# Kernel optimization log

Measured on AMD Instinct MI355X. Metric: run time of the kernel, lower is better.

Reference implementation:

```python
import jax, jax.numpy as jnp
import numpy as np

B, L, H = 2, 2048, 1024
N_HEADS = 16
HEAD = H // N_HEADS
LN_EPS = 1e-12


def setup_inputs() -> dict:
    key = jax.random.key(0)
    ks = jax.random.split(key, 8)
    s = 1.0 / np.sqrt(H)
    return {
        "embeddings": jax.random.normal(ks[0], (B, L, H), dtype=jnp.float32),
        "mask": jnp.zeros((B, 1, 1, L), dtype=jnp.float32),
        "Wq": jax.random.normal(ks[1], (H, H), dtype=jnp.float32) * s,
        "bq": jnp.zeros((H,), dtype=jnp.float32),
        "Wk": jax.random.normal(ks[2], (H, H), dtype=jnp.float32) * s,
        "bk": jnp.zeros((H,), dtype=jnp.float32),
        "Wv": jax.random.normal(ks[3], (H, H), dtype=jnp.float32) * s,
        "bv": jnp.zeros((H,), dtype=jnp.float32),
        "Wo": jax.random.normal(ks[4], (H, H), dtype=jnp.float32) * s,
        "bo": jnp.zeros((H,), dtype=jnp.float32),
        "ln_gamma": jnp.ones((H,), dtype=jnp.float32),
        "ln_beta": jnp.zeros((H,), dtype=jnp.float32),
    }


def _layer_norm(x, gamma, beta):
    mu = jnp.mean(x, axis=-1, keepdims=True)
    var = jnp.mean(jnp.square(x - mu), axis=-1, keepdims=True)
    return (x - mu) * jax.lax.rsqrt(var + LN_EPS) * gamma + beta


def reference(embeddings, mask, Wq, bq, Wk, bk, Wv, bv, Wo, bo, ln_gamma, ln_beta):
    b, l, h = embeddings.shape
    # QKV projections, split heads -> [b, n_heads, l, head]
    def split_heads(x):
        return x.reshape(b, l, N_HEADS, HEAD).transpose(0, 2, 1, 3)
    q = split_heads(embeddings @ Wq + bq)
    k = split_heads(embeddings @ Wk + bk)
    v = split_heads(embeddings @ Wv + bv)
    # Faithful to source: energies use Q @ V^T, scaled by sqrt(n_heads)
    energies = jnp.einsum("bhqd,bhkd->bhqk", q, v) / np.sqrt(N_HEADS) + mask
    weights = jax.nn.softmax(energies, axis=3)
    # Faithful to source: attended = weights @ K
    attended = jnp.einsum("bhqk,bhkd->bhqd", weights, k)
    attended = attended.transpose(0, 2, 1, 3).reshape(b, l, h)
    # Residual feed-forward (BertSelfOutput style): dense + residual + LN
    out = attended @ Wo + bo
    return _layer_norm(out + embeddings, ln_gamma, ln_beta)
```

## Files before the change

kernel.cpp:

```cpp
#include <hip/hip_runtime.h>

#define LOG2E 1.44269504f
#define C_QSCALE 0.360673760f
#define C_SHIFT  34.6246810f
typedef unsigned short u16;
typedef short bf16x8 __attribute__((ext_vector_type(8)));
typedef float f32x4 __attribute__((ext_vector_type(4)));
typedef unsigned short u16x4 __attribute__((ext_vector_type(4)));

#define BB 2
#define LL 2048
#define HH 1024
#define NH 16
#define HD 64
#define ML (BB*LL)

__device__ __forceinline__ u16 f2bf(float f) {
  union { float f; unsigned u; } v; v.f = f;
  unsigned r = v.u + 0x7FFFu + ((v.u >> 16) & 1u);
  return (u16)(r >> 16);
}
__device__ __forceinline__ u16 f2bf_trunc(float f) {
  union { float f; unsigned u; } v; v.f = f;
  return (u16)(v.u >> 16);
}
__device__ __forceinline__ float bf2f(u16 u) {
  union { unsigned u; float f; } v; v.u = ((unsigned)u) << 16;
  return v.f;
}
__device__ __forceinline__ void gload_lds16(const u16* g, u16* l) {
  __builtin_amdgcn_global_load_lds((const __attribute__((address_space(1))) void*)g,
                                   (__attribute__((address_space(3))) void*)l, 16, 0, 0);
}

__global__ __launch_bounds__(256) void k_prep(const float* __restrict__ E, u16* __restrict__ X,
                                              const float* W0, const float* W1,
                                              const float* W2, const float* W3,
                                              u16* __restrict__ WT) {
  __shared__ __align__(16) u16 T[64*72];
  if (blockIdx.x < 2048) {
    int idx = (blockIdx.x * 256 + threadIdx.x) * 8;
    float4 a = *(const float4*)(E + idx);
    float4 b = *(const float4*)(E + idx + 4);
    bf16x8 o;
    o[0]=f2bf(a.x); o[1]=f2bf(a.y); o[2]=f2bf(a.z); o[3]=f2bf(a.w);
    o[4]=f2bf(b.x); o[5]=f2bf(b.y); o[6]=f2bf(b.z); o[7]=f2bf(b.w);
    *(bf16x8*)(X + idx) = o;
    return;
  }
  int bz = blockIdx.x - 2048;
  int z = bz >> 8, rem = bz & 255, bx = rem & 15, by = rem >> 4;
  const float* W = (z==0)?W0:(z==1)?W1:(z==2)?W2:W3;
  u16* dst = WT + (size_t)z * HH * HH;
  int t = threadIdx.x;
  int n0 = bx * 64, k0 = by * 64;
  int kl = t >> 2, nc = t & 3;
  #pragma unroll
  for (int u = 0; u < 4; ++u) {
    float4 v = *(const float4*)(W + (size_t)(k0 + kl) * HH + n0 + nc*16 + u*4);
    int nb = nc*16 + u*4;
    T[(nb+0)*72 + kl] = f2bf(v.x);
    T[(nb+1)*72 + kl] = f2bf(v.y);
    T[(nb+2)*72 + kl] = f2bf(v.z);
    T[(nb+3)*72 + kl] = f2bf(v.w);
  }
  __syncthreads();
  int nl = t >> 2, kc = (t & 3) * 16;
  #pragma unroll
  for (int e = 0; e < 2; ++e) {
    bf16x8 v = *(const bf16x8*)(T + nl*72 + kc + e*8);
    *(bf16x8*)(dst + (size_t)(n0+nl)*HH + k0 + kc + e*8) = v;
  }
}

__global__ __launch_bounds__(256) void k_gemm(const u16* __restrict__ A, const u16* __restrict__ Bt,
                                              const float* __restrict__ b0, const float* __restrict__ b1,
                                              const float* __restrict__ b2,
                                              u16* __restrict__ QH, u16* __restrict__ KV) {
  __shared__ __align__(16) u16 As[2][128*32];
  __shared__ __align__(16) u16 Bs[2][128*32];
  int tid = threadIdx.x;
  int lane = tid & 63, w = tid >> 6;
  int c = lane & 15, g = lane >> 4;
  int bn0 = blockIdx.x * 128, bm0 = blockIdx.y * 128;
  int wm0 = (w >> 1) * 64, wn0 = (w & 1) * 64;
  int z = bn0 >> 10;
  bool swapd = (z != 1);
  const u16* srcA = swapd ? Bt : A;
  const u16* srcB = swapd ? A : Bt;
  int baseA = swapd ? bn0 : bm0;
  int baseB = swapd ? bm0 : bn0;

  f32x4 acc[4][4];
  #pragma unroll
  for (int mt = 0; mt < 4; ++mt)
    #pragma unroll
    for (int nt = 0; nt < 4; ++nt)
      acc[mt][nt] = (f32x4){0.f,0.f,0.f,0.f};

  #pragma unroll
  for (int it = 0; it < 2; ++it) {
    int ch = tid + it*256, row = ch >> 2, col = (ch & 3) * 8;
    gload_lds16(srcA + (size_t)(baseA + row) * HH + col, &As[0][ch*8]);
    gload_lds16(srcB + (size_t)(baseB + row) * HH + col, &Bs[0][ch*8]);
  }
  for (int kt = 0; kt < 32; ++kt) {
    __syncthreads();
    int cb = kt & 1;
    if (kt < 31) {
      int k0 = (kt + 1) * 32, nb = (kt + 1) & 1;
      #pragma unroll
      for (int it = 0; it < 2; ++it) {
        int ch = tid + it*256, row = ch >> 2, col = (ch & 3) * 8;
        gload_lds16(srcA + (size_t)(baseA + row) * HH + k0 + col, &As[nb][ch*8]);
        gload_lds16(srcB + (size_t)(baseB + row) * HH + k0 + col, &Bs[nb][ch*8]);
      }
    }
    bf16x8 af[4], bfr[4];
    #pragma unroll
    for (int i = 0; i < 4; ++i) {
      af[i]  = *(const bf16x8*)(&As[cb][0] + (wm0 + i*16 + c)*32 + g*8);
      bfr[i] = *(const bf16x8*)(&Bs[cb][0] + (wn0 + i*16 + c)*32 + g*8);
    }
    #pragma unroll
    for (int mt = 0; mt < 4; ++mt)
      #pragma unroll
      for (int nt = 0; nt < 4; ++nt)
        acc[mt][nt] = __builtin_amdgcn_mfma_f32_16x16x32_bf16(af[mt], bfr[nt], acc[mt][nt], 0, 0, 0);
  }

  if (z == 1) {
    #pragma unroll
    for (int nt = 0; nt < 4; ++nt) {
      int n = bn0 + wn0 + nt*16 + c;
      int nn = n & 1023, h = nn >> 6, d = nn & 63;
      float bv = b1[nn];
      #pragma unroll
      for (int mt = 0; mt < 4; ++mt) {
        int m0 = bm0 + wm0 + mt*16 + 4*g;
        int b = m0 >> 11, keyl = m0 & 2047;
        int tt = keyl >> 6, chunk = (keyl >> 3) & 7, s = keyl & 7;
        u16x4 pk;
        #pragma unroll
        for (int r = 0; r < 4; ++r) pk[r] = f2bf(acc[mt][nt][r] + bv);
        *(u16x4*)(KV + ((size_t)((b*NH + h)*32 + tt))*8192 + d*64 + ((chunk ^ (d & 7))*8) + s) = pk;
      }
    }
  } else {
    #pragma unroll
    for (int mt = 0; mt < 4; ++mt) {
      int nidx0 = bn0 + wm0 + mt*16 + 4*g;
      int nn0 = nidx0 & 1023, h = nn0 >> 6, d0 = nn0 & 63;
      const float* bp = (z == 0) ? b0 : b2;
      float4 bv = *(const float4*)(bp + nn0);
      #pragma unroll
      for (int nt = 0; nt < 4; ++nt) {
        int tok = bm0 + wn0 + nt*16 + c;
        int b = tok >> 11, l = tok & 2047;
        u16x4 o;
        o[0] = f2bf(acc[mt][nt][0] + bv.x);
        o[1] = f2bf(acc[mt][nt][1] + bv.y);
        o[2] = f2bf(acc[mt][nt][2] + bv.z);
        o[3] = f2bf(acc[mt][nt][3] + bv.w);
        if (z == 0) {
          *(u16x4*)(QH + (((size_t)(b*NH + h)) * LL + l) * HD + d0) = o;
        } else {
          int tt = l >> 6;
          *(u16x4*)(KV + ((size_t)((b*NH + h)*32 + tt))*8192 + 4096
                    + (l & 63)*64 + (((d0 >> 3) ^ (l & 7))*8) + (d0 & 7)) = o;
        }
      }
    }
  }
}

__global__ __launch_bounds__(256) void k_gemm_o(const u16* __restrict__ ATT, const u16* __restrict__ Wt,
                                                const float* __restrict__ bias,
                                                float* __restrict__ outf) {
  __shared__ __align__(16) u16 As[2][128*32];
  __shared__ __align__(16) u16 Bs[2][64*32];
  int tid = threadIdx.x;
  int lane = tid & 63, w = tid >> 6;
  int c = lane & 15, g = lane >> 4;
  int bn0 = blockIdx.x * 128, bm0 = blockIdx.y * 64;
  int wm0 = (w >> 1) * 64, wn0 = (w & 1) * 32;

  f32x4 acc[4][2];
  #pragma unroll
  for (int mt = 0; mt < 4; ++mt)
    #pragma unroll
    for (int nt = 0; nt < 2; ++nt)
      acc[mt][nt] = (f32x4){0.f,0.f,0.f,0.f};

  #pragma unroll
  for (int it = 0; it < 2; ++it) {
    int ch = tid + it*256, row = ch >> 2, col = (ch & 3) * 8;
    gload_lds16(Wt + (size_t)(bn0 + row) * HH + col, &As[0][ch*8]);
  }
  { int row = tid >> 2, col = (tid & 3) * 8;
    gload_lds16(ATT + (size_t)(bm0 + row) * HH + col, &Bs[0][tid*8]); }

  for (int kt = 0; kt < 32; ++kt) {
    __syncthreads();
    int cb = kt & 1;
    if (kt < 31) {
      int k0 = (kt + 1) * 32, nb = (kt + 1) & 1;
      #pragma unroll
      for (int it = 0; it < 2; ++it) {
        int ch = tid + it*256, row = ch >> 2, col = (ch & 3) * 8;
        gload_lds16(Wt + (size_t)(bn0 + row) * HH + k0 + col, &As[nb][ch*8]);
      }
      int row = tid >> 2, col = (tid & 3) * 8;
      gload_lds16(ATT + (size_t)(bm0 + row) * HH + k0 + col, &Bs[nb][tid*8]);
    }
    bf16x8 af[4], bfr[2];
    #pragma unroll
    for (int i = 0; i < 4; ++i)
      af[i] = *(const bf16x8*)(&As[cb][0] + (wm0 + i*16 + c)*32 + g*8);
    #pragma unroll
    for (int j = 0; j < 2; ++j)
      bfr[j] = *(const bf16x8*)(&Bs[cb][0] + (wn0 + j*16 + c)*32 + g*8);
    #pragma unroll
    for (int mt = 0; mt < 4; ++mt)
      #pragma unroll
      for (int nt = 0; nt < 2; ++nt)
        acc[mt][nt] = __builtin_amdgcn_mfma_f32_16x16x32_bf16(af[mt], bfr[nt], acc[mt][nt], 0, 0, 0);
  }
  #pragma unroll
  for (int mt = 0; mt < 4; ++mt) {
    int n0 = bn0 + wm0 + mt*16 + 4*g;
    float4 bv = *(const float4*)(bias + n0);
    #pragma unroll
    for (int nt = 0; nt < 2; ++nt) {
      int tok = bm0 + wn0 + nt*16 + c;
      float4 o;
      o.x = acc[mt][nt][0] + bv.x;
      o.y = acc[mt][nt][1] + bv.y;
      o.z = acc[mt][nt][2] + bv.z;
      o.w = acc[mt][nt][3] + bv.w;
      *(float4*)(outf + (size_t)tok * HH + n0) = o;
    }
  }
}

__global__ __launch_bounds__(256) void k_attn(const u16* __restrict__ QH, const u16* __restrict__ KV,
                                              const float* __restrict__ mask,
                                              u16* __restrict__ PO0, u16* __restrict__ PO1,
                                              u16* __restrict__ PO2, float* __restrict__ PL) {
  __shared__ __align__(16) u16 sKV[8192];
  __shared__ __align__(16) u16 sP[4][16*72];
  int tid = threadIdx.x;
  int lane = tid & 63, w = tid >> 6;
  int c = lane & 15, g = lane >> 4;
  int z = blockIdx.y;
  int bh = blockIdx.z, b = bh >> 4;
  int q0 = blockIdx.x * 128 + w * 32;
  size_t qbase = (size_t)bh * LL * HD;
  const u16* kvg = KV + (size_t)bh * 32 * 8192;
  const float* mptr = mask + b * LL;
  u16* pw = &sP[w][0];
  int t0 = (z < 2) ? z*11 : 22;
  int tn = (z < 2) ? 11 : 10;

  bf16x8 aq[2][2];
  #pragma unroll
  for (int qi = 0; qi < 2; ++qi)
    #pragma unroll
    for (int ks = 0; ks < 2; ++ks)
      aq[qi][ks] = *(const bf16x8*)(QH + qbase + (size_t)(q0 + qi*16 + c) * HD + ks*32 + g*8);

  bf16x8 ones;
  #pragma unroll
  for (int i = 0; i < 8; ++i) ones[i] = (short)0x3F80;

  f32x4 O[2][4], lac[2];
  #pragma unroll
  for (int qi = 0; qi < 2; ++qi) {
    lac[qi] = (f32x4){0.f,0.f,0.f,0.f};
    #pragma unroll
    for (int dt = 0; dt < 4; ++dt) O[qi][dt] = (f32x4){0.f,0.f,0.f,0.f};
  }

  for (int ti = 0; ti < tn; ++ti) {
    int t = t0 + ti;
    __syncthreads();
    #pragma unroll
    for (int it = 0; it < 4; ++it) {
      int i = (tid + it*256) * 8;
      gload_lds16(kvg + (size_t)t*8192 + i, sKV + i);
    }
    __syncthreads();

    int kv0 = t * 64;
    float mt4[4];
    #pragma unroll
    for (int nt = 0; nt < 4; ++nt)
      mt4[nt] = fmaf(mptr[kv0 + nt*16 + c], LOG2E, -C_SHIFT);

    #pragma unroll
    for (int qi = 0; qi < 2; ++qi) {
      #pragma unroll
      for (int nt = 0; nt < 4; ++nt) {
        int vrow = nt*16 + c;
        bf16x8 vb0 = *(const bf16x8*)(sKV + 4096 + vrow*64 + ((g ^ (c & 7))*8));
        bf16x8 vb1 = *(const bf16x8*)(sKV + 4096 + vrow*64 + (((4 + g) ^ (c & 7))*8));
        f32x4 sa = (f32x4){0.f,0.f,0.f,0.f};
        sa = __builtin_amdgcn_mfma_f32_16x16x32_bf16(aq[qi][0], vb0, sa, 0,0,0);
        sa = __builtin_amdgcn_mfma_f32_16x16x32_bf16(aq[qi][1], vb1, sa, 0,0,0);
        #pragma unroll
        for (int r = 0; r < 4; ++r)
          pw[(4*g + r)*72 + nt*16 + c] = f2bf_trunc(exp2f(fmaf(sa[r], C_QSCALE, mt4[nt])));
      }
      bf16x8 ap0 = *(const bf16x8*)(pw + c*72 + g*8);
      bf16x8 ap1 = *(const bf16x8*)(pw + c*72 + 32 + g*8);
      lac[qi] = __builtin_amdgcn_mfma_f32_16x16x32_bf16(ones, ap0, lac[qi], 0,0,0);
      lac[qi] = __builtin_amdgcn_mfma_f32_16x16x32_bf16(ones, ap1, lac[qi], 0,0,0);
      #pragma unroll
      for (int dt = 0; dt < 4; ++dt) {
        int d = dt*16 + c;
        bf16x8 bk0 = *(const bf16x8*)(sKV + d*64 + ((g ^ (c & 7))*8));
        bf16x8 bk1 = *(const bf16x8*)(sKV + d*64 + (((4 + g) ^ (c & 7))*8));
        O[qi][dt] = __builtin_amdgcn_mfma_f32_16x16x32_bf16(bk0, ap0, O[qi][dt], 0,0,0);
        O[qi][dt] = __builtin_amdgcn_mfma_f32_16x16x32_bf16(bk1, ap1, O[qi][dt], 0,0,0);
      }
    }
  }
  u16* POp = (z == 0) ? PO0 : (z == 1) ? PO1 : PO2;
  #pragma unroll
  for (int qi = 0; qi < 2; ++qi) {
    int q = q0 + qi*16 + c;
    size_t qrow = (size_t)bh * LL + q;
    if (g == 0) PL[(size_t)(z*32 + bh) * LL + q] = lac[qi][0];
    #pragma unroll
    for (int dt = 0; dt < 4; ++dt) {
      u16x4 o;
      #pragma unroll
      for (int r = 0; r < 4; ++r) o[r] = f2bf(O[qi][dt][r]);
      *(u16x4*)(POp + qrow*HD + dt*16 + 4*g) = o;
    }
  }
}

__global__ __launch_bounds__(256) void k_combine(const u16* __restrict__ PO0,
                                                 const u16* __restrict__ PO1,
                                                 const u16* __restrict__ PO2,
                                                 const float* __restrict__ PL,
                                                 u16* __restrict__ ATT) {
  int bh = blockIdx.y, b = bh >> 4, h = bh & 15;
  int q = blockIdx.x * 128 + (threadIdx.x >> 1);
  int dh = (threadIdx.x & 1) * 32;
  size_t r0 = ((size_t)bh * LL + q) * HD + dh;
  float inv = 1.0f / (PL[(size_t)bh * LL + q] + PL[(size_t)(32 + bh) * LL + q]
                    + PL[(size_t)(64 + bh) * LL + q]);
  u16* dst = ATT + ((size_t)(b*LL + q)) * HH + h*HD + dh;
  #pragma unroll
  for (int e = 0; e < 4; ++e) {
    bf16x8 a0 = *(const bf16x8*)(PO0 + r0 + e*8);
    bf16x8 a1 = *(const bf16x8*)(PO1 + r0 + e*8);
    bf16x8 a2 = *(const bf16x8*)(PO2 + r0 + e*8);
    bf16x8 o;
    #pragma unroll
    for (int i = 0; i < 8; ++i)
      o[i] = (short)f2bf((bf2f((u16)a0[i]) + bf2f((u16)a1[i]) + bf2f((u16)a2[i])) * inv);
    *(bf16x8*)(dst + e*8) = o;
  }
}

__global__ __launch_bounds__(256) void k_ln(const float* __restrict__ OF, const float* __restrict__ E,
                                            const float* __restrict__ gamma, const float* __restrict__ beta,
                                            float* __restrict__ out) {
  int row = blockIdx.x;
  int tid = threadIdx.x, lane = tid & 63, w = tid >> 6;
  size_t basei = (size_t)row * HH + tid*4;
  float4 a = *(const float4*)(OF + basei);
  float4 e = *(const float4*)(E + basei);
  float x0 = a.x + e.x, x1 = a.y + e.y, x2 = a.z + e.z, x3 = a.w + e.w;
  float s1 = x0+x1+x2+x3;
  float s2 = x0*x0+x1*x1+x2*x2+x3*x3;
  #pragma unroll
  for (int off = 32; off; off >>= 1) { s1 += __shfl_xor(s1, off); s2 += __shfl_xor(s2, off); }
  __shared__ float r1[4], r2[4];
  if (lane == 0) { r1[w] = s1; r2[w] = s2; }
  __syncthreads();
  s1 = r1[0]+r1[1]+r1[2]+r1[3];
  s2 = r2[0]+r2[1]+r2[2]+r2[3];
  float mu = s1 * (1.0f/HH);
  float var = s2 * (1.0f/HH) - mu*mu;
  float rs = rsqrtf(fmaxf(var, 0.f) + 1e-12f);
  int colb = tid*4;
  float4 gm = *(const float4*)(gamma + colb);
  float4 bt = *(const float4*)(beta + colb);
  float4 o;
  o.x = (x0-mu)*rs*gm.x + bt.x;
  o.y = (x1-mu)*rs*gm.y + bt.y;
  o.z = (x2-mu)*rs*gm.z + bt.z;
  o.w = (x3-mu)*rs*gm.w + bt.w;
  *(float4*)(out + basei) = o;
}

extern "C" void kernel_launch(void* const* d_in, const int* in_sizes, int n_in,
                              void* d_out, int out_size, void* d_ws, size_t ws_size,
                              hipStream_t stream) {
  const float* E    = (const float*)d_in[0];
  const float* mask = (const float*)d_in[1];
  const float* Wq   = (const float*)d_in[2];
  const float* bq   = (const float*)d_in[3];
  const float* Wk   = (const float*)d_in[4];
  const float* bk   = (const float*)d_in[5];
  const float* Wv   = (const float*)d_in[6];
  const float* bv   = (const float*)d_in[7];
  const float* Wo   = (const float*)d_in[8];
  const float* bo   = (const float*)d_in[9];
  const float* gam  = (const float*)d_in[10];
  const float* bet  = (const float*)d_in[11];

  const size_t MH = (size_t)ML * HH;
  u16* XBF = (u16*)d_ws;
  u16* WT  = XBF + MH;
  u16* QH  = WT + 4*(size_t)HH*HH;
  u16* KV  = QH + MH;
  u16* ATT = KV + 2*MH;
  u16* PO0 = ATT + MH;
  u16* PO1 = PO0 + MH;
  u16* PO2 = XBF;
  float* out = (float*)d_out;
  float* PL = out;
  float* OF = (float*)PO0;

  k_prep<<<dim3(3072), 256, 0, stream>>>(E, XBF, Wq, Wk, Wv, Wo, WT);
  k_gemm<<<dim3(24,32), 256, 0, stream>>>(XBF, WT, bq, bk, bv, QH, KV);
  k_attn<<<dim3(16,3,32), 256, 0, stream>>>(QH, KV, mask, PO0, PO1, PO2, PL);
  k_combine<<<dim3(16,32), 256, 0, stream>>>(PO0, PO1, PO2, PL, ATT);
  k_gemm_o<<<dim3(8,64), 256, 0, stream>>>(ATT, WT + 3*(size_t)HH*HH, bo, OF);
  k_ln<<<dim3(ML), 256, 0, stream>>>(OF, E, gam, bet, out);
}
```

Baseline: 253.6 us.

## Use 512-thread attention blocks with 256 queries and a 2-way KV split

Attention blocks now hold 8 waves covering 256 query rows, so each KV tile loaded into LDS is reused by twice as many queries. The KV split-K drops from 3 chunks to 2 (16 tiles each), which removes the third partial-output buffer and its read in the combine kernel. The grid shrinks from 1536 to 512 blocks, which lowers parallelism and makes each block's loop longer. The tighter launch bounds may also constrain register allocation.

New measurement: 313.6 us. +23.7%, slower.

```diff
diff --git a/kernel.cpp b/kernel.cpp
--- a/kernel.cpp
+++ b/kernel.cpp
@@ -243,24 +243,22 @@
   }
 }
 
-__global__ __launch_bounds__(256) void k_attn(const u16* __restrict__ QH, const u16* __restrict__ KV,
-                                              const float* __restrict__ mask,
-                                              u16* __restrict__ PO0, u16* __restrict__ PO1,
-                                              u16* __restrict__ PO2, float* __restrict__ PL) {
+__global__ __launch_bounds__(512, 8) void k_attn(const u16* __restrict__ QH, const u16* __restrict__ KV,
+                                                 const float* __restrict__ mask,
+                                                 u16* __restrict__ PO0, u16* __restrict__ PO1,
+                                                 float* __restrict__ PL) {
   __shared__ __align__(16) u16 sKV[8192];
-  __shared__ __align__(16) u16 sP[4][16*72];
+  __shared__ __align__(16) u16 sP[8][16*72];
   int tid = threadIdx.x;
   int lane = tid & 63, w = tid >> 6;
   int c = lane & 15, g = lane >> 4;
   int z = blockIdx.y;
   int bh = blockIdx.z, b = bh >> 4;
-  int q0 = blockIdx.x * 128 + w * 32;
+  int q0 = blockIdx.x * 256 + w * 32;
   size_t qbase = (size_t)bh * LL * HD;
-  const u16* kvg = KV + (size_t)bh * 32 * 8192;
-  const float* mptr = mask + b * LL;
+  const u16* kvg = KV + (size_t)bh * 32 * 8192 + (size_t)z * 16 * 8192;
+  const float* mptr = mask + b * LL + z * 1024;
   u16* pw = &sP[w][0];
-  int t0 = (z < 2) ? z*11 : 22;
-  int tn = (z < 2) ? 11 : 10;
 
   bf16x8 aq[2][2];
   #pragma unroll
@@ -281,17 +279,16 @@
     for (int dt = 0; dt < 4; ++dt) O[qi][dt] = (f32x4){0.f,0.f,0.f,0.f};
   }
 
-  for (int ti = 0; ti < tn; ++ti) {
-    int t = t0 + ti;
+  for (int tt = 0; tt < 16; ++tt) {
     __syncthreads();
     #pragma unroll
-    for (int it = 0; it < 4; ++it) {
-      int i = (tid + it*256) * 8;
-      gload_lds16(kvg + (size_t)t*8192 + i, sKV + i);
+    for (int it = 0; it < 2; ++it) {
+      int i = (tid + it*512) * 8;
+      gload_lds16(kvg + (size_t)tt*8192 + i, sKV + i);
     }
     __syncthreads();
 
-    int kv0 = t * 64;
+    int kv0 = tt * 64;
     float mt4[4];
     #pragma unroll
     for (int nt = 0; nt < 4; ++nt)
@@ -325,7 +322,7 @@
       }
     }
   }
-  u16* POp = (z == 0) ? PO0 : (z == 1) ? PO1 : PO2;
+  u16* POp = (z == 0) ? PO0 : PO1;
   #pragma unroll
   for (int qi = 0; qi < 2; ++qi) {
     int q = q0 + qi*16 + c;
@@ -343,25 +340,22 @@
 
 __global__ __launch_bounds__(256) void k_combine(const u16* __restrict__ PO0,
                                                  const u16* __restrict__ PO1,
-                                                 const u16* __restrict__ PO2,
                                                  const float* __restrict__ PL,
                                                  u16* __restrict__ ATT) {
   int bh = blockIdx.y, b = bh >> 4, h = bh & 15;
   int q = blockIdx.x * 128 + (threadIdx.x >> 1);
   int dh = (threadIdx.x & 1) * 32;
   size_t r0 = ((size_t)bh * LL + q) * HD + dh;
-  float inv = 1.0f / (PL[(size_t)bh * LL + q] + PL[(size_t)(32 + bh) * LL + q]
-                    + PL[(size_t)(64 + bh) * LL + q]);
+  float inv = 1.0f / (PL[(size_t)bh * LL + q] + PL[(size_t)(32 + bh) * LL + q]);
   u16* dst = ATT + ((size_t)(b*LL + q)) * HH + h*HD + dh;
   #pragma unroll
   for (int e = 0; e < 4; ++e) {
     bf16x8 a0 = *(const bf16x8*)(PO0 + r0 + e*8);
     bf16x8 a1 = *(const bf16x8*)(PO1 + r0 + e*8);
-    bf16x8 a2 = *(const bf16x8*)(PO2 + r0 + e*8);
     bf16x8 o;
     #pragma unroll
     for (int i = 0; i < 8; ++i)
-      o[i] = (short)f2bf((bf2f((u16)a0[i]) + bf2f((u16)a1[i]) + bf2f((u16)a2[i])) * inv);
+      o[i] = (short)f2bf((bf2f((u16)a0[i]) + bf2f((u16)a1[i])) * inv);
     *(bf16x8*)(dst + e*8) = o;
   }
 }
@@ -422,15 +416,14 @@
   u16* ATT = KV + 2*MH;
   u16* PO0 = ATT + MH;
   u16* PO1 = PO0 + MH;
-  u16* PO2 = XBF;
   float* out = (float*)d_out;
   float* PL = out;
   float* OF = (float*)PO0;
 
   k_prep<<<dim3(3072), 256, 0, stream>>>(E, XBF, Wq, Wk, Wv, Wo, WT);
   k_gemm<<<dim3(24,32), 256, 0, stream>>>(XBF, WT, bq, bk, bv, QH, KV);
-  k_attn<<<dim3(16,3,32), 256, 0, stream>>>(QH, KV, mask, PO0, PO1, PO2, PL);
-  k_combine<<<dim3(16,32), 256, 0, stream>>>(PO0, PO1, PO2, PL, ATT);
+  k_attn<<<dim3(8,2,32), 512, 0, stream>>>(QH, KV, mask, PO0, PO1, PL);
+  k_combine<<<dim3(16,32), 256, 0, stream>>>(PO0, PO1, PL, ATT);
   k_gemm_o<<<dim3(8,64), 256, 0, stream>>>(ATT, WT + 3*(size_t)HH*HH, bo, OF);
   k_ln<<<dim3(ML), 256, 0, stream>>>(OF, E, gam, bet, out);
 }
```
